# Kernel tuning notes

Hardware: AMD Instinct MI355X
Metric: run time of the kernel (lower is better)

Reference implementation:

```python
import jax, jax.numpy as jnp
import numpy as np

TOP_K = 2


def setup_inputs() -> dict:
    key = jax.random.key(0)
    ks = jax.random.split(key, 6)
    B, S, H, I, E = 2, 1024, 1024, 2048, 8
    s_h = 1.0 / np.sqrt(H)
    s_i = 1.0 / np.sqrt(I)
    return {
        "x": jax.random.normal(ks[0], (B, S, H), jnp.float32),
        "gate_w": jax.random.normal(ks[1], (H, E), jnp.float32) * s_h,
        "gate_b": jnp.zeros((E,), jnp.float32),
        "w1": jax.random.normal(ks[2], (E, H, I), jnp.float32) * s_h,
        "w3": jax.random.normal(ks[3], (E, H, I), jnp.float32) * s_h,
        "w2": jax.random.normal(ks[4], (E, I, H), jnp.float32) * s_i,
    }


def reference(x, gate_w, gate_b, w1, w3, w2):
    # Gating: softmax over experts, then top-k selection + renormalization.
    logits = jnp.einsum("bsh,he->bse", x, gate_w) + gate_b            # [B,S,E]
    probs = jax.nn.softmax(logits, axis=-1)
    topk_w, topk_idx = jax.lax.top_k(probs, TOP_K)                    # [B,S,K]
    topk_w = topk_w / jnp.sum(topk_w, axis=-1, keepdims=True)

    E = gate_w.shape[-1]
    # Per-token combine weight for each expert (0 if not routed there).
    # one_hot: [B,S,K,E] -> combine: [B,S,E]
    combine = jnp.sum(jax.nn.one_hot(topk_idx, E, dtype=x.dtype) * topk_w[..., None], axis=-2)

    # SwiGLU expert FFN: down(silu(gate(x)) * up(x)); dense-masked reference
    # (compute every expert on every token, weight by combine; math identical
    # to the original gather/scatter loop since combine is 0 off-route).
    out = jnp.zeros_like(x)
    for e in range(E):
        h = jax.nn.silu(x @ w1[e]) * (x @ w3[e])                      # [B,S,I]
        out = out + combine[..., e:e + 1] * (h @ w2[e])               # [B,S,H]
    return out
```

## Files before the change

kernel.cpp:

```cpp
#include <hip/hip_runtime.h>
#include <hip/hip_bf16.h>
#include <math.h>

typedef __attribute__((ext_vector_type(4))) float f32x4;
typedef __attribute__((ext_vector_type(8))) short bf16x8;

#define T_TOK 2048
#define H_DIM 1024
#define I_DIM 2048
#define E_NUM 8

__device__ inline unsigned short f2bf(float f) {
  union { float f; unsigned int u; } v; v.f = f;
  unsigned int r = v.u + 0x7fffu + ((v.u >> 16) & 1u);
  return (unsigned short)(r >> 16);
}
__device__ inline unsigned int pack2(float a, float b) {
  return (unsigned int)f2bf(a) | ((unsigned int)f2bf(b) << 16);
}

__device__ inline void gld16(const void* g, void* l) {
  __builtin_amdgcn_global_load_lds((const __attribute__((address_space(1))) void*)g,
                                   (__attribute__((address_space(3))) void*)l, 16, 0, 0);
}

__device__ inline void transpose_tile(const float* __restrict__ ip, unsigned short* __restrict__ op,
                                      int R, int C, int rt, int ct, char* smem)
{
  unsigned short (*tl)[66] = (unsigned short (*)[66])smem;
  int r0 = rt * 64, c0 = ct * 64;
  int tid = threadIdx.x;
  int rq = (tid >> 4) * 4;
  int c4 = (tid & 15) * 4;
  const float* base = ip + (size_t)(r0 + rq) * C + c0 + c4;
  float4 v0 = *(const float4*)(base);
  float4 v1 = *(const float4*)(base + C);
  float4 v2 = *(const float4*)(base + 2 * C);
  float4 v3 = *(const float4*)(base + 3 * C);
  const float* f0 = (const float*)&v0;
  const float* f1 = (const float*)&v1;
  const float* f2 = (const float*)&v2;
  const float* f3 = (const float*)&v3;
#pragma unroll
  for (int j = 0; j < 4; ++j) {
    *(unsigned int*)&tl[c4 + j][rq]     = pack2(f0[j], f1[j]);
    *(unsigned int*)&tl[c4 + j][rq + 2] = pack2(f2[j], f3[j]);
  }
  __syncthreads();
  int c = tid >> 3, r8 = (tid & 7) * 8;
#pragma unroll
  for (int it = 0; it < 2; ++it) {
    int cc = c + it * 32;
    uint4 o;
    o.x = *(const unsigned int*)&tl[cc][r8];
    o.y = *(const unsigned int*)&tl[cc][r8 + 2];
    o.z = *(const unsigned int*)&tl[cc][r8 + 4];
    o.w = *(const unsigned int*)&tl[cc][r8 + 6];
    *(uint4*)(op + (size_t)(c0 + cc) * R + r0 + r8) = o;
  }
}

__global__ __launch_bounds__(256) void gate_t13(
    const float* __restrict__ x, const float* __restrict__ gw, const float* __restrict__ gb,
    int* __restrict__ rec_e, float* __restrict__ rec_w, unsigned short* __restrict__ xb,
    const float* __restrict__ w1, const float* __restrict__ w3,
    unsigned short* __restrict__ w1t, unsigned short* __restrict__ w3t)
{
  __shared__ __align__(16) char smem[64 * 66 * 2];
  int bx = blockIdx.x;
  if (bx >= 512) {
    int idx = bx - 512;
    int m = idx >> 9;
    int t9 = idx & 511;
    int rt = t9 & 15;
    int ct = t9 >> 4;
    const float* ip = (m < 8 ? w1 : w3) + (size_t)(m & 7) * ((size_t)H_DIM * I_DIM);
    unsigned short* op = (m < 8 ? w1t : w3t) + (size_t)(m & 7) * ((size_t)H_DIM * I_DIM);
    transpose_tile(ip, op, H_DIM, I_DIM, rt, ct, smem);
    return;
  }
  int wv = threadIdx.x >> 6, lane = threadIdx.x & 63;
  int t = bx * 4 + wv;
  const float* xr = x + (size_t)t * H_DIM;
  unsigned short* xo = xb + (size_t)t * H_DIM;
  float acc[8];
#pragma unroll
  for (int e = 0; e < 8; ++e) acc[e] = 0.f;
  for (int i = 0; i < H_DIM / 64; ++i) {
    int h = i * 64 + lane;
    float xv = xr[h];
    xo[h] = f2bf(xv);
    const float4* g = (const float4*)(gw + (size_t)h * 8);
    float4 g0 = g[0], g1 = g[1];
    acc[0] += xv * g0.x; acc[1] += xv * g0.y; acc[2] += xv * g0.z; acc[3] += xv * g0.w;
    acc[4] += xv * g1.x; acc[5] += xv * g1.y; acc[6] += xv * g1.z; acc[7] += xv * g1.w;
  }
#pragma unroll
  for (int s = 1; s < 64; s <<= 1) {
#pragma unroll
    for (int e = 0; e < 8; ++e) acc[e] += __shfl_xor(acc[e], s);
  }
  if (lane == 0) {
    float l[8];
#pragma unroll
    for (int e = 0; e < 8; ++e) l[e] = acc[e] + gb[e];
    int e0 = 0;
    for (int e = 1; e < 8; ++e) if (l[e] > l[e0]) e0 = e;
    int e1 = (e0 == 0) ? 1 : 0;
    for (int e = 0; e < 8; ++e) if (e != e0 && l[e] > l[e1]) e1 = e;
    float w0 = 1.f / (1.f + expf(l[e1] - l[e0]));
    rec_e[t * 2]     = e0; rec_e[t * 2 + 1] = e1;
    rec_w[t * 2]     = w0; rec_w[t * 2 + 1] = 1.f - w0;
  }
}

__global__ __launch_bounds__(256) void route_kernel(
    const int* __restrict__ rec_e, const float* __restrict__ rec_w,
    int* __restrict__ counts_g, int* __restrict__ list_tok, float* __restrict__ list_w)
{
  __shared__ int cnt[8], base[8], fill[8];
  int tid = threadIdx.x;
  if (tid < 8) { cnt[tid] = 0; fill[tid] = 0; }
  __syncthreads();
  int e_loc[16];
  int c_loc[8];
#pragma unroll
  for (int e = 0; e < 8; ++e) c_loc[e] = 0;
#pragma unroll
  for (int it = 0; it < 16; ++it) {
    e_loc[it] = rec_e[it * 256 + tid];
    c_loc[e_loc[it] & 7]++;
  }
#pragma unroll
  for (int e = 0; e < 8; ++e) if (c_loc[e]) atomicAdd(&cnt[e], c_loc[e]);
  __syncthreads();
  if (tid == 0) {
    int b = 0;
    for (int e = 0; e < 8; ++e) { base[e] = b; b += cnt[e]; }
  }
  if (tid < 8) counts_g[tid] = cnt[tid];
  __syncthreads();
#pragma unroll
  for (int it = 0; it < 16; ++it) {
    int i = it * 256 + tid;
    int e = e_loc[it] & 7;
    int pos = atomicAdd(&fill[e], 1);
    list_tok[base[e] + pos] = i;
    list_w[base[e] + pos]   = rec_w[i];
  }
}

__global__ __launch_bounds__(256) void gemm1_t2(
    const unsigned short* __restrict__ xb,
    const unsigned short* __restrict__ w1t,
    const unsigned short* __restrict__ w3t,
    const int* __restrict__ counts,
    const int* __restrict__ list_tok,
    unsigned short* __restrict__ hbuf,
    const float* __restrict__ w2,
    unsigned short* __restrict__ w2t)
{
  __shared__ __align__(16) char smem[16384];
  int bx = blockIdx.x;
  if (bx >= 8192) {
    int idx = bx - 8192;
    int e = idx >> 9;
    int t9 = idx & 511;
    int rt = t9 & 31;
    int ct = t9 >> 5;
    const float* ip = w2 + (size_t)e * ((size_t)H_DIM * I_DIM);
    unsigned short* op = w2t + (size_t)e * ((size_t)H_DIM * I_DIM);
    transpose_tile(ip, op, I_DIM, H_DIM, rt, ct, smem);
    return;
  }
  int e = bx >> 10;
  int y = (bx >> 5) & 31;
  int ix = bx & 31;
  int nbase = 0;
#pragma unroll
  for (int i = 0; i < 8; ++i) if (i < e) nbase += counts[i];
  int n_e = counts[e];
  int t0 = y * 128;
  if (t0 >= n_e) return;
  int i0 = ix * 64;

  unsigned short* As  = (unsigned short*)smem;
  unsigned short* B1s = (unsigned short*)(smem + 8192);
  unsigned short* B3s = (unsigned short*)(smem + 12288);

  int tid = threadIdx.x;
  int r = tid >> 2;
  int seg = (tid & 3) * 8;

  int sr0 = t0 + r;       if (sr0 >= n_e) sr0 = n_e - 1;
  int sr1 = t0 + 64 + r;  if (sr1 >= n_e) sr1 = n_e - 1;
  int tok0 = list_tok[nbase + sr0] >> 1;
  int tok1 = list_tok[nbase + sr1] >> 1;
  const char* gA0 = (const char*)(xb + (size_t)tok0 * H_DIM + seg);
  const char* gA1 = (const char*)(xb + (size_t)tok1 * H_DIM + seg);
  const char* gB1 = (const char*)(w1t + ((size_t)e * I_DIM + i0 + r) * H_DIM + seg);
  const char* gB3 = (const char*)(w3t + ((size_t)e * I_DIM + i0 + r) * H_DIM + seg);

  char* lA0 = (char*)As + tid * 16;
  char* lA1 = (char*)As + 4096 + tid * 16;
  char* lB1 = (char*)B1s + tid * 16;
  char* lB3 = (char*)B3s + tid * 16;

  int w = tid >> 6, lane = tid & 63, lm = lane & 15, lq = lane >> 4;
  int wm = w & 1, wn = w >> 1;

  f32x4 acc1[4][2], acc3[4][2];
#pragma unroll
  for (int i = 0; i < 4; ++i)
#pragma unroll
    for (int j = 0; j < 2; ++j) { acc1[i][j] = (f32x4){0,0,0,0}; acc3[i][j] = (f32x4){0,0,0,0}; }

  for (int kb = 0; kb < H_DIM; kb += 32) {
    __syncthreads();
    gld16(gA0 + kb * 2, lA0);
    gld16(gA1 + kb * 2, lA1);
    gld16(gB1 + kb * 2, lB1);
    gld16(gB3 + kb * 2, lB3);
    __syncthreads();
    bf16x8 a[4], b1[2], b3[2];
#pragma unroll
    for (int i = 0; i < 4; ++i)
      a[i] = *(const bf16x8*)((const char*)As + 2 * ((wm * 64 + i * 16 + lm) * 32 + lq * 8));
#pragma unroll
    for (int j = 0; j < 2; ++j) {
      b1[j] = *(const bf16x8*)((const char*)B1s + 2 * ((wn * 32 + j * 16 + lm) * 32 + lq * 8));
      b3[j] = *(const bf16x8*)((const char*)B3s + 2 * ((wn * 32 + j * 16 + lm) * 32 + lq * 8));
    }
#pragma unroll
    for (int i = 0; i < 4; ++i)
#pragma unroll
      for (int j = 0; j < 2; ++j) {
        acc1[i][j] = __builtin_amdgcn_mfma_f32_16x16x32_bf16(a[i], b1[j], acc1[i][j], 0, 0, 0);
        acc3[i][j] = __builtin_amdgcn_mfma_f32_16x16x32_bf16(a[i], b3[j], acc3[i][j], 0, 0, 0);
      }
  }

#pragma unroll
  for (int i = 0; i < 4; ++i) {
#pragma unroll
    for (int rr = 0; rr < 4; ++rr) {
      int slot = t0 + wm * 64 + i * 16 + lq * 4 + rr;
      if (slot < n_e) {
#pragma unroll
        for (int j = 0; j < 2; ++j) {
          float g = acc1[i][j][rr], u = acc3[i][j][rr];
          float hv = (g / (1.f + __expf(-g))) * u;
          hbuf[(size_t)(nbase + slot) * I_DIM + i0 + wn * 32 + j * 16 + lm] = f2bf(hv);
        }
      }
    }
  }
}

__global__ __launch_bounds__(256) void gemm2(
    const unsigned short* __restrict__ hbuf,
    const unsigned short* __restrict__ w2t,
    const int* __restrict__ counts,
    const int* __restrict__ list_tok,
    const float* __restrict__ list_w,
    float* __restrict__ partial)
{
  int e = blockIdx.z;
  int nbase = 0;
#pragma unroll
  for (int i = 0; i < 8; ++i) if (i < e) nbase += counts[i];
  int n_e = counts[e];
  int ts = blockIdx.y >> 1, kh = blockIdx.y & 1;
  int t0 = ts * 64;
  if (t0 >= n_e) return;
  int h0 = blockIdx.x * 128;
  int k0 = kh * (I_DIM / 2);

  __shared__ __align__(16) unsigned short As[64 * 32];
  __shared__ __align__(16) unsigned short Bs[128 * 32];

  int tid = threadIdx.x;
  int r = tid >> 2;
  int seg = (tid & 3) * 8;

  int sr = t0 + r; if (sr >= n_e) sr = n_e - 1;
  const char* gA  = (const char*)(hbuf + (size_t)(nbase + sr) * I_DIM + k0 + seg);
  const char* gB0 = (const char*)(w2t + ((size_t)e * H_DIM + h0 + r) * I_DIM + k0 + seg);
  const char* gB1 = (const char*)(w2t + ((size_t)e * H_DIM + h0 + 64 + r) * I_DIM + k0 + seg);

  char* lA  = (char*)As + tid * 16;
  char* lB0 = (char*)Bs + tid * 16;
  char* lB1 = (char*)Bs + 4096 + tid * 16;

  int w = tid >> 6, lane = tid & 63, lm = lane & 15, lq = lane >> 4;
  int wm = w & 1, wn = (w >> 1) * 64;

  f32x4 acc[2][4];
#pragma unroll
  for (int i = 0; i < 2; ++i)
#pragma unroll
    for (int j = 0; j < 4; ++j) acc[i][j] = (f32x4){0,0,0,0};

  for (int kb = 0; kb < I_DIM / 2; kb += 32) {
    __syncthreads();
    gld16(gA + kb * 2, lA);
    gld16(gB0 + kb * 2, lB0);
    gld16(gB1 + kb * 2, lB1);
    __syncthreads();
    bf16x8 a[2], b[4];
#pragma unroll
    for (int i = 0; i < 2; ++i)
      a[i] = *(const bf16x8*)((const char*)As + 2 * ((wm * 32 + i * 16 + lm) * 32 + lq * 8));
#pragma unroll
    for (int j = 0; j < 4; ++j)
      b[j] = *(const bf16x8*)((const char*)Bs + 2 * ((wn + j * 16 + lm) * 32 + lq * 8));
#pragma unroll
    for (int i = 0; i < 2; ++i)
#pragma unroll
      for (int j = 0; j < 4; ++j)
        acc[i][j] = __builtin_amdgcn_mfma_f32_16x16x32_bf16(a[i], b[j], acc[i][j], 0, 0, 0);
  }

  int entv[2][4]; float wtv[2][4];
#pragma unroll
  for (int i = 0; i < 2; ++i)
#pragma unroll
    for (int rr = 0; rr < 4; ++rr) {
      int slot = t0 + wm * 32 + i * 16 + lq * 4 + rr;
      if (slot < n_e) { entv[i][rr] = list_tok[nbase + slot]; wtv[i][rr] = list_w[nbase + slot]; }
      else entv[i][rr] = -1;
    }
#pragma unroll
  for (int i = 0; i < 2; ++i)
#pragma unroll
    for (int j = 0; j < 4; ++j)
#pragma unroll
      for (int rr = 0; rr < 4; ++rr) {
        if (entv[i][rr] >= 0) {
          int t = entv[i][rr] >> 1, kk = entv[i][rr] & 1;
          int plane = kh * 2 + kk;
          partial[((size_t)plane * T_TOK + t) * H_DIM + h0 + wn + j * 16 + lm] =
              acc[i][j][rr] * wtv[i][rr];
        }
      }
}

__global__ __launch_bounds__(256) void combine4(const float* __restrict__ partial,
                                                float* __restrict__ out)
{
  const size_t P = (size_t)T_TOK * H_DIM;
  int i = (blockIdx.x * 256 + threadIdx.x) * 4;
  float4 a = *(const float4*)(partial + i);
  float4 b = *(const float4*)(partial + P + i);
  float4 c = *(const float4*)(partial + 2 * P + i);
  float4 d = *(const float4*)(partial + 3 * P + i);
  float4 o;
  o.x = a.x + b.x + c.x + d.x;
  o.y = a.y + b.y + c.y + d.y;
  o.z = a.z + b.z + c.z + d.z;
  o.w = a.w + b.w + c.w + d.w;
  *(float4*)(out + i) = o;
}

extern "C" void kernel_launch(void* const* d_in, const int* in_sizes, int n_in,
                              void* d_out, int out_size, void* d_ws, size_t ws_size,
                              hipStream_t stream) {
  const float* x  = (const float*)d_in[0];
  const float* gw = (const float*)d_in[1];
  const float* gb = (const float*)d_in[2];
  const float* w1 = (const float*)d_in[3];
  const float* w3 = (const float*)d_in[4];
  const float* w2 = (const float*)d_in[5];
  float* out = (float*)d_out;

  char* ws = (char*)d_ws;
  int*   counts   = (int*)(ws);
  int*   rec_e    = (int*)(ws + 128);
  float* rec_w    = (float*)(ws + 16512);
  int*   list_tok = (int*)(ws + 32896);
  float* list_w   = (float*)(ws + 49280);
  const size_t MB = 1024ull * 1024ull;
  unsigned short* xb   = (unsigned short*)(ws + 1 * MB);
  unsigned short* w1t  = (unsigned short*)(ws + 5 * MB);
  float* partial       = (float*)(ws + 5 * MB);
  unsigned short* w3t  = (unsigned short*)(ws + 37 * MB);
  unsigned short* w2t  = (unsigned short*)(ws + 69 * MB);
  unsigned short* hbuf = (unsigned short*)(ws + 101 * MB);

  gate_t13<<<512 + 8192, 256, 0, stream>>>(x, gw, gb, rec_e, rec_w, xb, w1, w3, w1t, w3t);
  route_kernel<<<1, 256, 0, stream>>>(rec_e, rec_w, counts, list_tok, list_w);
  gemm1_t2<<<8192 + 4096, 256, 0, stream>>>(xb, w1t, w3t, counts, list_tok, hbuf, w2, w2t);
  gemm2<<<dim3(H_DIM / 128, 128, E_NUM), 256, 0, stream>>>(hbuf, w2t, counts, list_tok, list_w, partial);
  combine4<<<(T_TOK * H_DIM) / (256 * 4), 256, 0, stream>>>(partial, out);
}
```

Before: 349.7 us.

## Widen gemm1 tile, split gemm2 K four ways, parallelize routing per expert

The gate/up GEMM now computes a 128-wide intermediate tile per block instead of 64. Each gathered token tile is loaded half as often, at the cost of more accumulator registers and a launch bound of 2 blocks per CU. The down-projection GEMM splits K into four chunks instead of two, which doubles its grid but writes 8 partial planes, so the final combine must read 8 planes instead of 4. Routing list construction moves from a single block to one block per expert, each scanning all records and appending only its own expert's entries.

```diff
diff --git a/kernel.cpp b/kernel.cpp
--- a/kernel.cpp
+++ b/kernel.cpp
@@ -114,43 +114,45 @@
   }
 }
 
-__global__ __launch_bounds__(256) void route_kernel(
+__global__ __launch_bounds__(256) void route8(
     const int* __restrict__ rec_e, const float* __restrict__ rec_w,
     int* __restrict__ counts_g, int* __restrict__ list_tok, float* __restrict__ list_w)
 {
-  __shared__ int cnt[8], base[8], fill[8];
+  __shared__ int cnt[8];
+  __shared__ int fill;
+  int e = blockIdx.x;
   int tid = threadIdx.x;
-  if (tid < 8) { cnt[tid] = 0; fill[tid] = 0; }
+  if (tid < 8) cnt[tid] = 0;
+  if (tid == 0) fill = 0;
   __syncthreads();
   int e_loc[16];
   int c_loc[8];
 #pragma unroll
-  for (int e = 0; e < 8; ++e) c_loc[e] = 0;
+  for (int k = 0; k < 8; ++k) c_loc[k] = 0;
 #pragma unroll
   for (int it = 0; it < 16; ++it) {
-    e_loc[it] = rec_e[it * 256 + tid];
-    c_loc[e_loc[it] & 7]++;
-  }
-#pragma unroll
-  for (int e = 0; e < 8; ++e) if (c_loc[e]) atomicAdd(&cnt[e], c_loc[e]);
+    e_loc[it] = rec_e[it * 256 + tid] & 7;
+    c_loc[e_loc[it]]++;
+  }
+#pragma unroll
+  for (int k = 0; k < 8; ++k) if (c_loc[k]) atomicAdd(&cnt[k], c_loc[k]);
   __syncthreads();
-  if (tid == 0) {
-    int b = 0;
-    for (int e = 0; e < 8; ++e) { base[e] = b; b += cnt[e]; }
-  }
-  if (tid < 8) counts_g[tid] = cnt[tid];
-  __syncthreads();
+  if (e == 0 && tid < 8) counts_g[tid] = cnt[tid];
+  int base = 0;
+#pragma unroll
+  for (int k = 0; k < 8; ++k) if (k < e) base += cnt[k];
 #pragma unroll
   for (int it = 0; it < 16; ++it) {
-    int i = it * 256 + tid;
-    int e = e_loc[it] & 7;
-    int pos = atomicAdd(&fill[e], 1);
-    list_tok[base[e] + pos] = i;
-    list_w[base[e] + pos]   = rec_w[i];
-  }
-}
-
-__global__ __launch_bounds__(256) void gemm1_t2(
+    if (e_loc[it] == e) {
+      int i = it * 256 + tid;
+      int pos = atomicAdd(&fill, 1);
+      list_tok[base + pos] = i;
+      list_w[base + pos]   = rec_w[i];
+    }
+  }
+}
+
+__global__ __launch_bounds__(256, 2) void gemm1_t2(
     const unsigned short* __restrict__ xb,
     const unsigned short* __restrict__ w1t,
     const unsigned short* __restrict__ w3t,
@@ -160,10 +162,10 @@
     const float* __restrict__ w2,
     unsigned short* __restrict__ w2t)
 {
-  __shared__ __align__(16) char smem[16384];
+  __shared__ __align__(16) char smem[24576];
   int bx = blockIdx.x;
-  if (bx >= 8192) {
-    int idx = bx - 8192;
+  if (bx >= 4096) {
+    int idx = bx - 4096;
     int e = idx >> 9;
     int t9 = idx & 511;
     int rt = t9 & 31;
@@ -173,68 +175,74 @@
     transpose_tile(ip, op, I_DIM, H_DIM, rt, ct, smem);
     return;
   }
-  int e = bx >> 10;
-  int y = (bx >> 5) & 31;
-  int ix = bx & 31;
+  int e = bx >> 9;
+  int y = (bx >> 4) & 31;
+  int ix = bx & 15;
   int nbase = 0;
 #pragma unroll
   for (int i = 0; i < 8; ++i) if (i < e) nbase += counts[i];
   int n_e = counts[e];
   int t0 = y * 128;
   if (t0 >= n_e) return;
-  int i0 = ix * 64;
+  int i0 = ix * 128;
 
   unsigned short* As  = (unsigned short*)smem;
   unsigned short* B1s = (unsigned short*)(smem + 8192);
-  unsigned short* B3s = (unsigned short*)(smem + 12288);
+  unsigned short* B3s = (unsigned short*)(smem + 16384);
 
   int tid = threadIdx.x;
-  int r = tid >> 2;
+  int r4 = tid >> 2;
   int seg = (tid & 3) * 8;
 
-  int sr0 = t0 + r;       if (sr0 >= n_e) sr0 = n_e - 1;
-  int sr1 = t0 + 64 + r;  if (sr1 >= n_e) sr1 = n_e - 1;
+  int sr0 = t0 + r4;       if (sr0 >= n_e) sr0 = n_e - 1;
+  int sr1 = t0 + 64 + r4;  if (sr1 >= n_e) sr1 = n_e - 1;
   int tok0 = list_tok[nbase + sr0] >> 1;
   int tok1 = list_tok[nbase + sr1] >> 1;
   const char* gA0 = (const char*)(xb + (size_t)tok0 * H_DIM + seg);
   const char* gA1 = (const char*)(xb + (size_t)tok1 * H_DIM + seg);
-  const char* gB1 = (const char*)(w1t + ((size_t)e * I_DIM + i0 + r) * H_DIM + seg);
-  const char* gB3 = (const char*)(w3t + ((size_t)e * I_DIM + i0 + r) * H_DIM + seg);
-
-  char* lA0 = (char*)As + tid * 16;
-  char* lA1 = (char*)As + 4096 + tid * 16;
-  char* lB1 = (char*)B1s + tid * 16;
-  char* lB3 = (char*)B3s + tid * 16;
+  const char* gB1a = (const char*)(w1t + ((size_t)e * I_DIM + i0 + r4) * H_DIM + seg);
+  const char* gB1b = (const char*)(w1t + ((size_t)e * I_DIM + i0 + 64 + r4) * H_DIM + seg);
+  const char* gB3a = (const char*)(w3t + ((size_t)e * I_DIM + i0 + r4) * H_DIM + seg);
+  const char* gB3b = (const char*)(w3t + ((size_t)e * I_DIM + i0 + 64 + r4) * H_DIM + seg);
+
+  char* lA0  = (char*)As + tid * 16;
+  char* lA1  = (char*)As + 4096 + tid * 16;
+  char* lB1a = (char*)B1s + tid * 16;
+  char* lB1b = (char*)B1s + 4096 + tid * 16;
+  char* lB3a = (char*)B3s + tid * 16;
+  char* lB3b = (char*)B3s + 4096 + tid * 16;
 
   int w = tid >> 6, lane = tid & 63, lm = lane & 15, lq = lane >> 4;
   int wm = w & 1, wn = w >> 1;
 
-  f32x4 acc1[4][2], acc3[4][2];
+  f32x4 acc1[4][4], acc3[4][4];
 #pragma unroll
   for (int i = 0; i < 4; ++i)
 #pragma unroll
-    for (int j = 0; j < 2; ++j) { acc1[i][j] = (f32x4){0,0,0,0}; acc3[i][j] = (f32x4){0,0,0,0}; }
+    for (int j = 0; j < 4; ++j) { acc1[i][j] = (f32x4){0,0,0,0}; acc3[i][j] = (f32x4){0,0,0,0}; }
 
   for (int kb = 0; kb < H_DIM; kb += 32) {
     __syncthreads();
     gld16(gA0 + kb * 2, lA0);
     gld16(gA1 + kb * 2, lA1);
-    gld16(gB1 + kb * 2, lB1);
-    gld16(gB3 + kb * 2, lB3);
+    gld16(gB1a + kb * 2, lB1a);
+    gld16(gB1b + kb * 2, lB1b);
+    gld16(gB3a + kb * 2, lB3a);
+    gld16(gB3b + kb * 2, lB3b);
     __syncthreads();
-    bf16x8 a[4], b1[2], b3[2];
+    bf16x8 a[4], b1[4], b3[4];
 #pragma unroll
     for (int i = 0; i < 4; ++i)
       a[i] = *(const bf16x8*)((const char*)As + 2 * ((wm * 64 + i * 16 + lm) * 32 + lq * 8));
 #pragma unroll
-    for (int j = 0; j < 2; ++j) {
-      b1[j] = *(const bf16x8*)((const char*)B1s + 2 * ((wn * 32 + j * 16 + lm) * 32 + lq * 8));
-      b3[j] = *(const bf16x8*)((const char*)B3s + 2 * ((wn * 32 + j * 16 + lm) * 32 + lq * 8));
+    for (int j = 0; j < 4; ++j) {
+      b1[j] = *(const bf16x8*)((const char*)B1s + 2 * ((wn * 64 + j * 16 + lm) * 32 + lq * 8));
+      b3[j] = *(const bf16x8*)((const char*)B3s + 2 * ((wn * 64 + j * 16 + lm) * 32 + lq * 8));
     }
 #pragma unroll
     for (int i = 0; i < 4; ++i)
 #pragma unroll
-      for (int j = 0; j < 2; ++j) {
+      for (int j = 0; j < 4; ++j) {
         acc1[i][j] = __builtin_amdgcn_mfma_f32_16x16x32_bf16(a[i], b1[j], acc1[i][j], 0, 0, 0);
         acc3[i][j] = __builtin_amdgcn_mfma_f32_16x16x32_bf16(a[i], b3[j], acc3[i][j], 0, 0, 0);
       }
@@ -246,11 +254,12 @@
     for (int rr = 0; rr < 4; ++rr) {
       int slot = t0 + wm * 64 + i * 16 + lq * 4 + rr;
       if (slot < n_e) {
-#pragma unroll
-        for (int j = 0; j < 2; ++j) {
+        unsigned short* orow = hbuf + (size_t)(nbase + slot) * I_DIM + i0 + wn * 64 + lm;
+#pragma unroll
+        for (int j = 0; j < 4; ++j) {
           float g = acc1[i][j][rr], u = acc3[i][j][rr];
           float hv = (g / (1.f + __expf(-g))) * u;
-          hbuf[(size_t)(nbase + slot) * I_DIM + i0 + wn * 32 + j * 16 + lm] = f2bf(hv);
+          orow[j * 16] = f2bf(hv);
         }
       }
     }
@@ -270,11 +279,11 @@
 #pragma unroll
   for (int i = 0; i < 8; ++i) if (i < e) nbase += counts[i];
   int n_e = counts[e];
-  int ts = blockIdx.y >> 1, kh = blockIdx.y & 1;
+  int ts = blockIdx.y >> 2, kh = blockIdx.y & 3;
   int t0 = ts * 64;
   if (t0 >= n_e) return;
   int h0 = blockIdx.x * 128;
-  int k0 = kh * (I_DIM / 2);
+  int k0 = kh * (I_DIM / 4);
 
   __shared__ __align__(16) unsigned short As[64 * 32];
   __shared__ __align__(16) unsigned short Bs[128 * 32];
@@ -301,7 +310,7 @@
 #pragma unroll
     for (int j = 0; j < 4; ++j) acc[i][j] = (f32x4){0,0,0,0};
 
-  for (int kb = 0; kb < I_DIM / 2; kb += 32) {
+  for (int kb = 0; kb < I_DIM / 4; kb += 32) {
     __syncthreads();
     gld16(gA + kb * 2, lA);
     gld16(gB0 + kb * 2, lB0);
@@ -345,21 +354,18 @@
       }
 }
 
-__global__ __launch_bounds__(256) void combine4(const float* __restrict__ partial,
+__global__ __launch_bounds__(256) void combine8(const float* __restrict__ partial,
                                                 float* __restrict__ out)
 {
   const size_t P = (size_t)T_TOK * H_DIM;
-  int i = (blockIdx.x * 256 + threadIdx.x) * 4;
-  float4 a = *(const float4*)(partial + i);
-  float4 b = *(const float4*)(partial + P + i);
-  float4 c = *(const float4*)(partial + 2 * P + i);
-  float4 d = *(const float4*)(partial + 3 * P + i);
-  float4 o;
-  o.x = a.x + b.x + c.x + d.x;
-  o.y = a.y + b.y + c.y + d.y;
-  o.z = a.z + b.z + c.z + d.z;
-  o.w = a.w + b.w + c.w + d.w;
-  *(float4*)(out + i) = o;
+  size_t i = (size_t)(blockIdx.x * 256 + threadIdx.x) * 4;
+  float4 s = *(const float4*)(partial + i);
+#pragma unroll
+  for (int p = 1; p < 8; ++p) {
+    float4 v = *(const float4*)(partial + p * P + i);
+    s.x += v.x; s.y += v.y; s.z += v.z; s.w += v.w;
+  }
+  *(float4*)(out + i) = s;
 }
 
 extern "C" void kernel_launch(void* const* d_in, const int* in_sizes, int n_in,
@@ -388,8 +394,8 @@
   unsigned short* hbuf = (unsigned short*)(ws + 101 * MB);
 
   gate_t13<<<512 + 8192, 256, 0, stream>>>(x, gw, gb, rec_e, rec_w, xb, w1, w3, w1t, w3t);
-  route_kernel<<<1, 256, 0, stream>>>(rec_e, rec_w, counts, list_tok, list_w);
-  gemm1_t2<<<8192 + 4096, 256, 0, stream>>>(xb, w1t, w3t, counts, list_tok, hbuf, w2, w2t);
-  gemm2<<<dim3(H_DIM / 128, 128, E_NUM), 256, 0, stream>>>(hbuf, w2t, counts, list_tok, list_w, partial);
-  combine4<<<(T_TOK * H_DIM) / (256 * 4), 256, 0, stream>>>(partial, out);
-}
+  route8<<<8, 256, 0, stream>>>(rec_e, rec_w, counts, list_tok, list_w);
+  gemm1_t2<<<4096 + 4096, 256, 0, stream>>>(xb, w1t, w3t, counts, list_tok, hbuf, w2, w2t);
+  gemm2<<<dim3(H_DIM / 128, 256, E_NUM), 256, 0, stream>>>(hbuf, w2t, counts, list_tok, list_w, partial);
+  combine8<<<(T_TOK * H_DIM) / (256 * 4), 256, 0, stream>>>(partial, out);
+}
```

New measurement: 348.0 us. Within noise of the previous version (-0.5%).
